# Kernel optimization log

Hardware: AMD Instinct MI355X
Metric: run time of the kernel (lower is better)

Reference implementation:

```python
import jax, jax.numpy as jnp
import numpy as np

R, DIL = 3, 2  # radius, dilation for neighbor correlation


def conv2d(x, w, b):
    # standard 3x3 stride-1 SAME conv, NCHW / OIHW
    y = jax.lax.conv_general_dilated(x, w, (1, 1), 'SAME',
                                     dimension_numbers=('NCHW', 'OIHW', 'NCHW'))
    return y + b[None, :, None, None]


def bilinear_gather(x, py, px):
    # x: (n,c,h,w); py/px: (n,K,h,w) float sampling coords; zero outside bounds
    n, c, h, w = x.shape
    y0 = jnp.floor(py); x0 = jnp.floor(px)
    wy = py - y0; wx = px - x0
    xf = x.reshape(n, c, h * w)

    def gather(yi, xi):
        valid = ((yi >= 0) & (yi < h) & (xi >= 0) & (xi < w)).astype(x.dtype)
        yc = jnp.clip(yi, 0, h - 1).astype(jnp.int32)
        xc = jnp.clip(xi, 0, w - 1).astype(jnp.int32)
        idx = (yc * w + xc).reshape(n, -1)  # (n, K*h*w)
        v = jax.vmap(lambda f, i: f[:, i])(xf, idx)  # (n, c, K*h*w)
        return v.reshape(n, c, *yi.shape[1:]) * valid[:, None]

    v00 = gather(y0, x0); v01 = gather(y0, x0 + 1)
    v10 = gather(y0 + 1, x0); v11 = gather(y0 + 1, x0 + 1)
    wy_ = wy[:, None]; wx_ = wx[:, None]
    return (v00 * (1 - wy_) * (1 - wx_) + v01 * (1 - wy_) * wx_
            + v10 * wy_ * (1 - wx_) + v11 * wy_ * wx_)


def dcn(x, w, b, ow, ob):
    # DCNv2-style modulated deformable 3x3 conv, stride 1, pad 1, 1 deformable group.
    # Offset/mask predicted by an internal conv: channels = [dy(9), dx(9), mask(9)].
    n, c, h, w_ = x.shape
    K = 9
    om = conv2d(x, ow, ob)  # (n, 27, h, w)
    dy, dx = om[:, :K], om[:, K:2 * K]
    mask = jax.nn.sigmoid(om[:, 2 * K:])
    ky, kx = jnp.meshgrid(jnp.arange(-1, 2), jnp.arange(-1, 2), indexing='ij')
    ky = ky.reshape(K).astype(x.dtype); kx = kx.reshape(K).astype(x.dtype)
    yy = jnp.arange(h, dtype=x.dtype)[None, None, :, None]
    xx = jnp.arange(w_, dtype=x.dtype)[None, None, None, :]
    py = yy + ky[None, :, None, None] + dy  # (n,K,h,w)
    px = xx + kx[None, :, None, None] + dx
    samp = bilinear_gather(x, py, px) * mask[:, None]  # (n,c,K,h,w)
    return jnp.einsum('nckhw,ock->nohw', samp, w.reshape(w.shape[0], c, K)) + b[None, :, None, None]


def ncf(f1, f2, radius, dilation):
    # neighbor_correlation_filter: unfold-based sliding-window dot-product attention
    n, c, h, w = f2.shape
    k = 2 * radius + 1
    pad = (k - 1) * dilation // 2
    f2p = jnp.pad(f2, ((0, 0), (0, 0), (pad, pad), (pad, pad)))
    # (n,c,K,h,w), tap order (ky outer, kx inner) matching F.unfold row-major layout
    patches = jnp.stack([f2p[:, :, i * dilation:i * dilation + h, j * dilation:j * dilation + w]
                         for i in range(k) for j in range(k)], axis=2)
    corr = jnp.einsum('nchw,nckhw->nkhw', f1, patches) / jnp.sqrt(jnp.asarray(c, f1.dtype))
    attn = jax.nn.softmax(corr, axis=1)
    sample = jnp.einsum('nkhw,nckhw->nchw', attn, patches)
    return sample, corr


def stargru(x, t, zw, zb, zow, zob, hw, hb, how, hob):
    tx = jnp.concatenate([x, t], axis=1)
    z = jax.nn.sigmoid(dcn(tx, zw, zb, zow, zob))
    r, _ = ncf(t, x, R, DIL)
    xt = jnp.tanh(dcn(jnp.concatenate([r, t], axis=1), hw, hb, how, hob))
    return (1.0 - z) * t + z * xt


def setup_inputs():
    key = jax.random.key(0)
    N, CIN, CH, H, W = 2, 256, 64, 96, 96
    ks = iter(jax.random.split(key, 32))

    def rn(shape, s=0.05):
        return jax.random.normal(next(ks), shape, jnp.float32) * s

    inp = {
        'x': jax.random.normal(next(ks), (N, CIN, H, W), jnp.float32),
        'template': jax.random.normal(next(ks), (N, CH, H, W), jnp.float32),
        'w_in': rn((CH, CIN, 3, 3)), 'b_in': jnp.zeros((CH,), jnp.float32),
        'w_out': rn((CIN, CH, 3, 3)), 'b_out': jnp.zeros((CIN,), jnp.float32),
    }
    for pre in ('enh_z', 'enh_h', 'upd_z', 'upd_h'):
        inp[pre + '_w'] = rn((CH, 2 * CH, 3, 3))
        inp[pre + '_b'] = jnp.zeros((CH,), jnp.float32)
        inp[pre + '_ow'] = rn((27, 2 * CH, 3, 3), 0.01)  # offset/mask conv (small init)
        inp[pre + '_ob'] = jnp.zeros((27,), jnp.float32)
    return inp


def reference(x, template, w_in, b_in, w_out, b_out,
              enh_z_w, enh_z_b, enh_z_ow, enh_z_ob,
              enh_h_w, enh_h_b, enh_h_ow, enh_h_ob,
              upd_z_w, upd_z_b, upd_z_ow, upd_z_ob,
              upd_h_w, upd_h_b, upd_h_ow, upd_h_ob):
    # CrossUpdate forward, post-first-frame branch (self.template is not None)
    xh = conv2d(x, w_in, b_in)
    x_enh = stargru(template, xh,
                    enh_z_w, enh_z_b, enh_z_ow, enh_z_ob,
                    enh_h_w, enh_h_b, enh_h_ow, enh_h_ob)
    new_template = stargru(xh, template,
                           upd_z_w, upd_z_b, upd_z_ow, upd_z_ob,
                           upd_h_w, upd_h_b, upd_h_ow, upd_h_ob)
    out = conv2d(x_enh, w_out, b_out)
    return (out, new_template)
```

## Files before the change

### kernel.cpp

```cpp
#include <hip/hip_runtime.h>
#include <hip/hip_bf16.h>

typedef __hip_bfloat16 bf16;
typedef unsigned short u16;
typedef unsigned int u32;
typedef __attribute__((ext_vector_type(8))) short short8;
typedef __attribute__((ext_vector_type(4))) short bh4;
typedef __attribute__((ext_vector_type(4))) float floatx4;

constexpr int N_ = 2, H_ = 96, W_ = 96, HW_ = H_ * W_;
constexpr int CIN_ = 256, CH_ = 64, C2_ = 128;

__device__ __forceinline__ float sigm(float v) { return 1.0f / (1.0f + __expf(-v)); }
__device__ __forceinline__ short f2b(float v) { bf16 h = __float2bfloat16(v); return *reinterpret_cast<short*>(&h); }
__device__ __forceinline__ float b2f(short s) {
    union { u32 i; float f; } v; v.i = ((u32)(u16)s) << 16; return v.f;
}

constexpr int A_IN_OFF = 0,                         A_IN_SZ  = 64 * 2304;
constexpr int A_OUT_OFF = A_IN_OFF + A_IN_SZ,       A_OUT_SZ = 256 * 576;
constexpr int A_OFF_OFF = A_OUT_OFF + A_OUT_SZ,     A_OFF_SZ = 64 * 1152;
constexpr int A_DCN_OFF = A_OFF_OFF + 4 * A_OFF_SZ, A_DCN_SZ = 64 * 1152;
constexpr int A_TOT = A_DCN_OFF + 4 * A_DCN_SZ;

__global__ __launch_bounds__(256) void cvt_weights(
        const float* __restrict__ w_in, const float* __restrict__ w_out,
        const float* __restrict__ ow0, const float* __restrict__ ow1,
        const float* __restrict__ ow2, const float* __restrict__ ow3,
        const float* __restrict__ w0, const float* __restrict__ w1,
        const float* __restrict__ w2, const float* __restrict__ w3,
        u16* __restrict__ dst) {
    int id = blockIdx.x * 256 + threadIdx.x;
    if (id >= A_TOT) return;
    float v;
    if (id < A_OUT_OFF) {
        int l = id; int m = l / 2304, k = l % 2304; int tap = k >> 8, ic = k & 255;
        v = w_in[m * 2304 + ic * 9 + tap];
    } else if (id < A_OFF_OFF) {
        int l = id - A_OUT_OFF; int m = l / 576, k = l % 576; int tap = k / 64, ic = k & 63;
        v = w_out[m * 576 + ic * 9 + tap];
    } else if (id < A_DCN_OFF) {
        int l = id - A_OFF_OFF; int i = l / A_OFF_SZ, l2 = l % A_OFF_SZ;
        int m = l2 / 1152, k = l2 % 1152; int tap = k >> 7, ic = k & 127;
        const float* s = (i == 0) ? ow0 : (i == 1) ? ow1 : (i == 2) ? ow2 : ow3;
        v = (m < 27) ? s[m * 1152 + ic * 9 + tap] : 0.f;
    } else {
        int l = id - A_DCN_OFF; int i = l / A_DCN_SZ, l2 = l % A_DCN_SZ;
        int m = l2 / 1152, k = l2 % 1152; int tap = k >> 7, c = k & 127;
        const float* s = (i == 0) ? w0 : (i == 1) ? w1 : (i == 2) ? w2 : w3;
        v = s[m * 1152 + c * 9 + tap];
    }
    short sb = f2b(v);
    dst[id] = *reinterpret_cast<u16*>(&sb);
}

__global__ __launch_bounds__(256) void prep(const float* __restrict__ x, const float* __restrict__ tpl,
                                            u16* __restrict__ xT, u16* __restrict__ ta, u16* __restrict__ tb) {
    int id = blockIdx.x * 256 + threadIdx.x;
    constexpr int XIDS = N_ * HW_ * 32;
    if (id < XIDS) {
        int c8 = id & 31;
        int pix = id >> 5;
        int n = pix / HW_, p = pix % HW_;
        const float* s = x + ((size_t)n * 256 + c8 * 8) * HW_ + p;
        short8 vv;
#pragma unroll
        for (int j = 0; j < 8; ++j) vv[j] = f2b(s[(size_t)j * HW_]);
        *reinterpret_cast<short8*>(xT + (size_t)pix * 256 + c8 * 8) = vv;
    } else {
        int id2 = id - XIDS;
        int c8 = id2 & 7;
        int pix = id2 >> 3;
        int n = pix / HW_, p = pix % HW_;
        const float* s = tpl + ((size_t)n * 64 + c8 * 8) * HW_ + p;
        short8 vv;
#pragma unroll
        for (int j = 0; j < 8; ++j) vv[j] = f2b(s[(size_t)j * HW_]);
        *reinterpret_cast<short8*>(ta + (size_t)pix * 128 + c8 * 8) = vv;
        *reinterpret_cast<short8*>(tb + (size_t)pix * 128 + 64 + c8 * 8) = vv;
    }
}

template <int IC, int OCST, int CC>
__device__ __forceinline__ void conv_core(const u16* __restrict__ X,
                                          const u16* __restrict__ A,
                                          const float* __restrict__ bias,
                                          float* __restrict__ out,
                                          u16* __restrict__ ta, u16* __restrict__ tb,
                                          int r, int mt, int t) {
    constexpr int K = IC * 9;
    constexpr int ICC = IC / 64;
    __shared__ __align__(16) u16 Xl[3][50][72];
    int n = r / 192;
    int rr = r % 192;
    int y = rr >> 1, px0 = (rr & 1) * 48;
    int w = t >> 6, lane = t & 63, lm = lane & 15, q = lane >> 4;
    const u16* Arow = A + (size_t)(mt * 64 + w * 16 + lm) * K + q * 8;
    floatx4 acc[3];
#pragma unroll
    for (int a = 0; a < 3; ++a) acc[a] = {0.f, 0.f, 0.f, 0.f};
    const short8 zz = {0, 0, 0, 0, 0, 0, 0, 0};

    for (int icc = 0; icc < ICC; ++icc) {
        short8 af[9][2];
#pragma unroll
        for (int tap = 0; tap < 9; ++tap)
#pragma unroll
            for (int ks = 0; ks < 2; ++ks)
                af[tap][ks] = *reinterpret_cast<const short8*>(Arow + tap * IC + icc * 64 + ks * 32);
        __syncthreads();
#pragma unroll
        for (int it = 0; it < 5; ++it) {
            int id = it * 256 + t;
            if (id < 1200) {
                int ch8 = id & 7;
                int tmp = id >> 3;
                int pxl = tmp % 50, row = tmp / 50;
                int xg = px0 - 1 + pxl;
                int yg = y - 1 + row;
                bool vld = (yg >= 0) && (yg < 96) && (xg >= 0) && (xg < 96);
                short8 vv = zz;
                if (vld)
                    vv = *reinterpret_cast<const short8*>(
                        X + ((size_t)(n * HW_ + yg * 96 + xg)) * IC + icc * 64 + ch8 * 8);
                *reinterpret_cast<short8*>(&Xl[row][pxl][ch8 * 8]) = vv;
            }
        }
        __syncthreads();
#pragma unroll
        for (int tap = 0; tap < 9; ++tap) {
            int ky = tap / 3, kx = tap % 3;
#pragma unroll
            for (int ks = 0; ks < 2; ++ks) {
#pragma unroll
                for (int nf = 0; nf < 3; ++nf) {
                    short8 bv = *reinterpret_cast<const short8*>(&Xl[ky][nf * 16 + lm + kx][ks * 32 + q * 8]);
                    acc[nf] = __builtin_amdgcn_mfma_f32_16x16x32_bf16(af[tap][ks], bv, acc[nf], 0, 0, 0);
                }
            }
        }
    }
    int ocb = mt * 64 + w * 16 + q * 4;
#pragma unroll
    for (int nf = 0; nf < 3; ++nf) {
        int px = px0 + nf * 16 + lm;
        if constexpr (CC) {
            int pix = n * HW_ + y * 96 + px;
            bh4 bo;
#pragma unroll
            for (int rr2 = 0; rr2 < 4; ++rr2) {
                int oc = ocb + rr2;
                float v = acc[nf][rr2] + bias[oc];
                out[((size_t)(n * OCST + oc)) * HW_ + y * 96 + px] = v;
                bo[rr2] = f2b(v);
            }
            *reinterpret_cast<bh4*>(ta + (size_t)pix * 128 + 64 + ocb) = bo;
            *reinterpret_cast<bh4*>(tb + (size_t)pix * 128 + ocb) = bo;
        } else {
#pragma unroll
            for (int rr2 = 0; rr2 < 4; ++rr2) {
                int oc = ocb + rr2;
                if (oc < OCST)
                    out[((size_t)(n * OCST + oc)) * HW_ + y * 96 + px] = acc[nf][rr2] + bias[oc];
            }
        }
    }
}

template <int IC, int OCST, int CC>
__global__ __launch_bounds__(256) void conv_gemm(const u16* __restrict__ X,
                                                 const u16* __restrict__ A,
                                                 const float* __restrict__ bias,
                                                 float* __restrict__ out,
                                                 u16* __restrict__ ta, u16* __restrict__ tb) {
    int cpx = gridDim.x >> 3;
    int b = (blockIdx.x & 7) * cpx + (blockIdx.x >> 3);
    conv_core<IC, OCST, CC>(X, A, bias, out, ta, tb, b % 384, b / 384, threadIdx.x);
}

template <int GATE>
__global__ __launch_bounds__(256) void od_fused(
        const u16* __restrict__ X0, const u16* __restrict__ X1,
        const u16* __restrict__ Ao0, const u16* __restrict__ Ao1,
        const float* __restrict__ bo0, const float* __restrict__ bo1,
        const u16* __restrict__ Ad0, const u16* __restrict__ Ad1,
        const float* __restrict__ bd0, const float* __restrict__ bd1,
        float* __restrict__ o0, float* __restrict__ o1,
        const float* __restrict__ g0, const float* __restrict__ g1,
        const float* __restrict__ t0, const float* __restrict__ t1,
        u16* __restrict__ xeh, float* __restrict__ ontpl) {
    __shared__ __align__(16) u16 Xl[3][50][72];
    __shared__ float om_l[27][48];
    __shared__ __align__(16) u16 Bl[2][48][72];
    __shared__ float s_wy[432], s_wx[432], s_m[432];
    __shared__ int s_y0[432], s_x0[432];

    int bid = blockIdx.x;
    int b = (bid & 7) * 96 + (bid >> 3);
    int inst = b / 384, r = b % 384, t = threadIdx.x;
    const u16* X = inst ? X1 : X0;
    const u16* Ao = inst ? Ao1 : Ao0;
    const float* bo = inst ? bo1 : bo0;
    const u16* Ad = inst ? Ad1 : Ad0;
    const float* bd = inst ? bd1 : bd0;
    int n = r / 192, rr = r % 192;
    int y = rr >> 1, px0 = (rr & 1) * 48;
    int w = t >> 6, lane = t & 63, lm = lane & 15, q = lane >> 4;
    const short8 zz = {0, 0, 0, 0, 0, 0, 0, 0};

    {
        const u16* Arow = Ao + (size_t)(w * 16 + lm) * 1152 + q * 8;
        floatx4 acc[3];
#pragma unroll
        for (int a = 0; a < 3; ++a) acc[a] = {0.f, 0.f, 0.f, 0.f};
        for (int icc = 0; icc < 2; ++icc) {
            short8 af[9][2];
#pragma unroll
            for (int tap = 0; tap < 9; ++tap)
#pragma unroll
                for (int ks = 0; ks < 2; ++ks)
                    af[tap][ks] = *reinterpret_cast<const short8*>(Arow + tap * 128 + icc * 64 + ks * 32);
            __syncthreads();
#pragma unroll
            for (int it = 0; it < 5; ++it) {
                int id = it * 256 + t;
                if (id < 1200) {
                    int ch8 = id & 7;
                    int tmp = id >> 3;
                    int pxl = tmp % 50, row = tmp / 50;
                    int xg = px0 - 1 + pxl;
                    int yg = y - 1 + row;
                    bool vld = (yg >= 0) && (yg < 96) && (xg >= 0) && (xg < 96);
                    short8 vv = zz;
                    if (vld)
                        vv = *reinterpret_cast<const short8*>(
                            X + ((size_t)(n * HW_ + yg * 96 + xg)) * 128 + icc * 64 + ch8 * 8);
                    *reinterpret_cast<short8*>(&Xl[row][pxl][ch8 * 8]) = vv;
                }
            }
            __syncthreads();
#pragma unroll
            for (int tap = 0; tap < 9; ++tap) {
                int ky = tap / 3, kx = tap % 3;
#pragma unroll
                for (int ks = 0; ks < 2; ++ks) {
#pragma unroll
                    for (int nf = 0; nf < 3; ++nf) {
                        short8 bv = *reinterpret_cast<const short8*>(&Xl[ky][nf * 16 + lm + kx][ks * 32 + q * 8]);
                        acc[nf] = __builtin_amdgcn_mfma_f32_16x16x32_bf16(af[tap][ks], bv, acc[nf], 0, 0, 0);
                    }
                }
            }
        }
        int ocb = w * 16 + q * 4;
#pragma unroll
        for (int nf = 0; nf < 3; ++nf) {
            int xl = nf * 16 + lm;
#pragma unroll
            for (int rr2 = 0; rr2 < 4; ++rr2) {
                int oc = ocb + rr2;
                if (oc < 27) om_l[oc][xl] = acc[nf][rr2] + bo[oc];
            }
        }
    }
    __syncthreads();

    for (int e = t; e < 432; e += 256) {
        int k9 = e / 48, xl = e % 48;
        int x = px0 + xl;
        float dy = om_l[k9][xl];
        float dx = om_l[9 + k9][xl];
        float ml = om_l[18 + k9][xl];
        float py = (float)y + (float)(k9 / 3 - 1) + dy;
        float px = (float)x + (float)(k9 % 3 - 1) + dx;
        float fy = floorf(py), fx = floorf(px);
        s_y0[e] = (int)fy; s_x0[e] = (int)fx;
        s_wy[e] = py - fy; s_wx[e] = px - fx; s_m[e] = sigm(ml);
    }
    __syncthreads();

    const u16* Arow = Ad + (size_t)(w * 16 + lm) * 1152 + q * 8;
    floatx4 acc[3];
#pragma unroll
    for (int a = 0; a < 3; ++a) acc[a] = {0.f, 0.f, 0.f, 0.f};
    const u16* txn = X + (size_t)n * HW_ * 128;
    int p = 0;
    bool active = (t < 192);
    short8 cA[4], cB[4];
    short8 afP[2];

    auto issueI = [&](int kc_, int id, short8* cr) {
        int tap = kc_ >> 1, c0 = (kc_ & 1) * 64;
        int px = id >> 3, ch8 = id & 7;
        int ce = tap * 48 + px;
        int y0 = s_y0[ce], x0c = s_x0[ce];
        bool yv0 = (y0 >= 0) & (y0 < 96), yv1 = (y0 >= -1) & (y0 < 95);
        bool xv0 = (x0c >= 0) & (x0c < 96), xv1 = (x0c >= -1) & (x0c < 95);
        const u16* gb = txn + (long)(y0 * 96 + x0c) * 128 + c0 + ch8 * 8;
        cr[0] = (yv0 && xv0) ? *reinterpret_cast<const short8*>(gb) : zz;
        cr[1] = (yv0 && xv1) ? *reinterpret_cast<const short8*>(gb + 128) : zz;
        cr[2] = (yv1 && xv0) ? *reinterpret_cast<const short8*>(gb + 96 * 128) : zz;
        cr[3] = (yv1 && xv1) ? *reinterpret_cast<const short8*>(gb + 96 * 128 + 128) : zz;
    };
    auto computeI = [&](int kc_, int id, const short8* cr) {
        int tap = kc_ >> 1;
        int px = id >> 3, ch8 = id & 7;
        int ce = tap * 48 + px;
        float wy = s_wy[ce], wx = s_wx[ce], m = s_m[ce];
        float w00 = (1.f - wy) * (1.f - wx) * m;
        float w01 = (1.f - wy) * wx * m;
        float w10 = wy * (1.f - wx) * m;
        float w11 = wy * wx * m;
        short8 vv;
#pragma unroll
        for (int j = 0; j < 8; ++j) {
            float f = b2f(cr[0][j]) * w00 + b2f(cr[1][j]) * w01 +
                      b2f(cr[2][j]) * w10 + b2f(cr[3][j]) * w11;
            vv[j] = f2b(f);
        }
        *reinterpret_cast<short8*>(&Bl[p][px][ch8 * 8]) = vv;
    };

    if (active) { issueI(0, t, cA); issueI(0, t + 192, cB); }
    for (int kc = 0; kc < 18; ++kc) {
        if (kc > 0) {
#pragma unroll
            for (int ks = 0; ks < 2; ++ks)
#pragma unroll
                for (int nf = 0; nf < 3; ++nf) {
                    short8 bv = *reinterpret_cast<const short8*>(&Bl[p ^ 1][nf * 16 + lm][ks * 32 + q * 8]);
                    acc[nf] = __builtin_amdgcn_mfma_f32_16x16x32_bf16(afP[ks], bv, acc[nf], 0, 0, 0);
                }
        }
        if (active) {
            computeI(kc, t, cA);
            computeI(kc, t + 192, cB);
            if (kc < 17) { issueI(kc + 1, t, cA); issueI(kc + 1, t + 192, cB); }
        }
#pragma unroll
        for (int ks = 0; ks < 2; ++ks)
            afP[ks] = *reinterpret_cast<const short8*>(Arow + kc * 64 + ks * 32);
        __syncthreads();
        p ^= 1;
    }
#pragma unroll
    for (int ks = 0; ks < 2; ++ks)
#pragma unroll
        for (int nf = 0; nf < 3; ++nf) {
            short8 bv = *reinterpret_cast<const short8*>(&Bl[p ^ 1][nf * 16 + lm][ks * 32 + q * 8]);
            acc[nf] = __builtin_amdgcn_mfma_f32_16x16x32_bf16(afP[ks], bv, acc[nf], 0, 0, 0);
        }

    int ocb = w * 16 + q * 4;
    if constexpr (GATE == 0) {
        float* out = inst ? o1 : o0;
#pragma unroll
        for (int nf = 0; nf < 3; ++nf) {
            int px = px0 + nf * 16 + lm;
#pragma unroll
            for (int rr2 = 0; rr2 < 4; ++rr2) {
                int oc = ocb + rr2;
                out[((size_t)(n * CH_ + oc)) * HW_ + y * 96 + px] = acc[nf][rr2] + bd[oc];
            }
        }
    } else {
        const float* gz = inst ? g1 : g0;
        const float* tt = inst ? t1 : t0;
#pragma unroll
        for (int nf = 0; nf < 3; ++nf) {
            int px = px0 + nf * 16 + lm;
            if (!inst) {
                bh4 bo4;
#pragma unroll
                for (int rr2 = 0; rr2 < 4; ++rr2) {
                    int oc = ocb + rr2;
                    size_t idx = ((size_t)(n * CH_ + oc)) * HW_ + y * 96 + px;
                    float z = sigm(gz[idx]);
                    float xt = tanhf(acc[nf][rr2] + bd[oc]);
                    bo4[rr2] = f2b((1.f - z) * tt[idx] + z * xt);
                }
                *reinterpret_cast<bh4*>(xeh + ((size_t)(n * HW_ + y * 96 + px)) * 64 + ocb) = bo4;
            } else {
#pragma unroll
                for (int rr2 = 0; rr2 < 4; ++rr2) {
                    int oc = ocb + rr2;
                    size_t idx = ((size_t)(n * CH_ + oc)) * HW_ + y * 96 + px;
                    float z = sigm(gz[idx]);
                    float xt = tanhf(acc[nf][rr2] + bd[oc]);
                    ontpl[idx] = (1.f - z) * tt[idx] + z * xt;
                }
            }
        }
    }
}

__global__ __launch_bounds__(256, 4) void ncf2(const u16* __restrict__ in0, const u16* __restrict__ in1,
                                               u16* __restrict__ out0, u16* __restrict__ out1) {
    __shared__ __align__(16) u16 sF2[7][28][72];
    __shared__ __align__(16) u16 sF1[16][72];
    __shared__ float sc[16][52];
    int t = threadIdx.x;
    int bid = blockIdx.x;
    int b = (bid & 7) * 288 + (bid >> 3);
    int inst = b / 1152, bb = b % 1152;
    const u16* txh = inst ? in1 : in0;
    u16* txh2 = inst ? out1 : out0;
    int n = bb / 576, rem = bb % 576;
    int y = rem / 6, x0 = (rem % 6) * 16;
    const u16* base = txh + (size_t)n * HW_ * 128;
    const short8 zz = {0, 0, 0, 0, 0, 0, 0, 0};

    for (int id = t; id < 1568; id += 256) {
        int ch8 = id & 7;
        int tmp = id >> 3;
        int px = tmp % 28, row = tmp / 28;
        int yy = y + row * 2 - 6;
        int xg = x0 - 6 + px;
        short8 vv = zz;
        if (yy >= 0 && yy < 96 && xg >= 0 && xg < 96)
            vv = *reinterpret_cast<const short8*>(base + (size_t)(yy * 96 + xg) * 128 + ch8 * 8);
        *reinterpret_cast<short8*>(&sF2[row][px][ch8 * 8]) = vv;
    }
    if (t < 128) {
        int ch8 = t & 7, lp0 = t >> 3;
        short8 vv = *reinterpret_cast<const short8*>(base + (size_t)(y * 96 + x0 + lp0) * 128 + 64 + ch8 * 8);
        *reinterpret_cast<short8*>(&sF1[lp0][ch8 * 8]) = vv;
    }
    __syncthreads();

    int lp = t >> 4, j = t & 15;
    for (int k = j; k < 49; k += 16) {
        int ky = k / 7, kx = k % 7;
        const u16* f2p = &sF2[ky][lp + 2 * kx][0];
        const u16* f1p = &sF1[lp][0];
        float s = 0.f;
#pragma unroll
        for (int c8 = 0; c8 < 8; ++c8) {
            short8 a = *reinterpret_cast<const short8*>(f1p + c8 * 8);
            short8 b2 = *reinterpret_cast<const short8*>(f2p + c8 * 8);
#pragma unroll
            for (int u = 0; u < 8; ++u) s += b2f(a[u]) * b2f(b2[u]);
        }
        sc[lp][k] = s * 0.125f;
    }
    float mx = -1e30f;
    for (int k = j; k < 49; k += 16) mx = fmaxf(mx, sc[lp][k]);
#pragma unroll
    for (int m = 1; m <= 8; m <<= 1) mx = fmaxf(mx, __shfl_xor(mx, m, 64));
    float e[4];
    float sum = 0.f;
    int cnt = 0;
    for (int k = j; k < 49; k += 16) { e[cnt] = __expf(sc[lp][k] - mx); sum += e[cnt]; ++cnt; }
#pragma unroll
    for (int m = 1; m <= 8; m <<= 1) sum += __shfl_xor(sum, m, 64);
    float inv = 1.f / sum;
    cnt = 0;
    for (int k = j; k < 49; k += 16) sc[lp][k] = e[cnt++] * inv;
    __syncthreads();
    int ch0 = j * 4;
    float acc[4];
#pragma unroll
    for (int u = 0; u < 4; ++u) acc[u] = 0.f;
#pragma unroll
    for (int k = 0; k < 49; ++k) {
        int ky = k / 7, kx = k % 7;
        float a = sc[lp][k];
        bh4 f2 = *reinterpret_cast<const bh4*>(&sF2[ky][lp + 2 * kx][ch0]);
#pragma unroll
        for (int u = 0; u < 4; ++u) acc[u] += a * b2f(f2[u]);
    }
    int p = y * 96 + x0 + lp;
    u16* obase = txh2 + (size_t)n * HW_ * 128 + (size_t)p * 128;
    bh4 ro;
#pragma unroll
    for (int u = 0; u < 4; ++u) ro[u] = f2b(acc[u]);
    *reinterpret_cast<bh4*>(obase + ch0) = ro;
    *reinterpret_cast<bh4*>(obase + 64 + ch0) =
        *reinterpret_cast<const bh4*>(&sF1[lp][ch0]);
}

extern "C" void kernel_launch(void* const* d_in, const int* in_sizes, int n_in,
                              void* d_out, int out_size, void* d_ws, size_t ws_size,
                              hipStream_t stream) {
    const float* x     = (const float*)d_in[0];
    const float* tpl   = (const float*)d_in[1];
    const float* w_in  = (const float*)d_in[2];
    const float* b_in  = (const float*)d_in[3];
    const float* w_out = (const float*)d_in[4];
    const float* b_out = (const float*)d_in[5];
    const float *pw[4], *pb[4], *pow_[4], *pob[4];
    for (int i = 0; i < 4; ++i) {
        pw[i]   = (const float*)d_in[6 + 4 * i];
        pb[i]   = (const float*)d_in[7 + 4 * i];
        pow_[i] = (const float*)d_in[8 + 4 * i];
        pob[i]  = (const float*)d_in[9 + 4 * i];
    }
    float* out_main = (float*)d_out;
    float* out_ntpl = out_main + (size_t)N_ * CIN_ * HW_;

    u16* Aws = (u16*)d_ws;
    u16* xT     = Aws + A_TOT;
    u16* txh_a  = xT + (size_t)N_ * HW_ * CIN_;
    u16* txh_b  = txh_a + (size_t)N_ * HW_ * C2_;
    u16* txh2_a = txh_b + (size_t)N_ * HW_ * C2_;
    u16* txh2_b = txh2_a + (size_t)N_ * HW_ * C2_;
    u16* xeh    = txh2_b + (size_t)N_ * HW_ * C2_;
    float* fws = (float*)(xeh + (size_t)N_ * HW_ * CH_);
    size_t off = 0;
    float* xh   = fws + off; off += (size_t)N_ * CH_ * HW_;
    float* dz_a = fws + off; off += (size_t)N_ * CH_ * HW_;
    float* dz_b = fws + off; off += (size_t)N_ * CH_ * HW_;

    cvt_weights<<<(A_TOT + 255) / 256, 256, 0, stream>>>(
        w_in, w_out, pow_[0], pow_[1], pow_[2], pow_[3], pw[0], pw[1], pw[2], pw[3], Aws);
    prep<<<2880, 256, 0, stream>>>(x, tpl, xT, txh_a, txh_b);
    conv_gemm<CIN_, 64, 1><<<384, 256, 0, stream>>>(xT, Aws + A_IN_OFF, b_in, xh, txh_a, txh_b);

    od_fused<0><<<768, 256, 0, stream>>>(txh_a, txh_b,
        Aws + A_OFF_OFF + 0 * A_OFF_SZ, Aws + A_OFF_OFF + 2 * A_OFF_SZ, pob[0], pob[2],
        Aws + A_DCN_OFF + 0 * A_DCN_SZ, Aws + A_DCN_OFF + 2 * A_DCN_SZ, pb[0], pb[2],
        dz_a, dz_b, nullptr, nullptr, nullptr, nullptr, nullptr, nullptr);

    ncf2<<<2304, 256, 0, stream>>>(txh_a, txh_b, txh2_a, txh2_b);

    od_fused<1><<<768, 256, 0, stream>>>(txh2_a, txh2_b,
        Aws + A_OFF_OFF + 1 * A_OFF_SZ, Aws + A_OFF_OFF + 3 * A_OFF_SZ, pob[1], pob[3],
        Aws + A_DCN_OFF + 1 * A_DCN_SZ, Aws + A_DCN_OFF + 3 * A_DCN_SZ, pb[1], pb[3],
        nullptr, nullptr, dz_a, dz_b, xh, tpl, xeh, out_ntpl);

    conv_gemm<CH_, 256, 0><<<1536, 256, 0, stream>>>(xeh, Aws + A_OUT_OFF, b_out, out_main, nullptr, nullptr);
}
```

Before: 310.6 us.

## Shrink pixel tile to 32 to raise block count and alias shared memory

Changes the per-block pixel tile from 48 to 32 pixels in the conv and fused offset/DCN kernels, raising grid sizes by half so more blocks spread across the CUs. In od_fused, the shared buffers are merged into one aliased allocation (the conv-stage input tile and the later B tile share storage), which lowers LDS use per block and can raise occupancy. All 256 threads now take part in the bilinear gather instead of 192 with two items each. The cost is more halo reloads and more weight-fragment reloads per output pixel.

```diff
diff --git a/kernel.cpp b/kernel.cpp
--- a/kernel.cpp
+++ b/kernel.cpp
@@ -90,15 +90,15 @@
                                           int r, int mt, int t) {
     constexpr int K = IC * 9;
     constexpr int ICC = IC / 64;
-    __shared__ __align__(16) u16 Xl[3][50][72];
-    int n = r / 192;
-    int rr = r % 192;
-    int y = rr >> 1, px0 = (rr & 1) * 48;
+    __shared__ __align__(16) u16 Xl[3][34][72];
+    int n = r / 288;
+    int rr = r % 288;
+    int y = rr / 3, px0 = (rr % 3) * 32;
     int w = t >> 6, lane = t & 63, lm = lane & 15, q = lane >> 4;
     const u16* Arow = A + (size_t)(mt * 64 + w * 16 + lm) * K + q * 8;
-    floatx4 acc[3];
-#pragma unroll
-    for (int a = 0; a < 3; ++a) acc[a] = {0.f, 0.f, 0.f, 0.f};
+    floatx4 acc[2];
+#pragma unroll
+    for (int a = 0; a < 2; ++a) acc[a] = {0.f, 0.f, 0.f, 0.f};
     const short8 zz = {0, 0, 0, 0, 0, 0, 0, 0};
 
     for (int icc = 0; icc < ICC; ++icc) {
@@ -110,12 +110,12 @@
                 af[tap][ks] = *reinterpret_cast<const short8*>(Arow + tap * IC + icc * 64 + ks * 32);
         __syncthreads();
 #pragma unroll
-        for (int it = 0; it < 5; ++it) {
+        for (int it = 0; it < 4; ++it) {
             int id = it * 256 + t;
-            if (id < 1200) {
+            if (id < 816) {
                 int ch8 = id & 7;
                 int tmp = id >> 3;
-                int pxl = tmp % 50, row = tmp / 50;
+                int pxl = tmp % 34, row = tmp / 34;
                 int xg = px0 - 1 + pxl;
                 int yg = y - 1 + row;
                 bool vld = (yg >= 0) && (yg < 96) && (xg >= 0) && (xg < 96);
@@ -133,7 +133,7 @@
 #pragma unroll
             for (int ks = 0; ks < 2; ++ks) {
 #pragma unroll
-                for (int nf = 0; nf < 3; ++nf) {
+                for (int nf = 0; nf < 2; ++nf) {
                     short8 bv = *reinterpret_cast<const short8*>(&Xl[ky][nf * 16 + lm + kx][ks * 32 + q * 8]);
                     acc[nf] = __builtin_amdgcn_mfma_f32_16x16x32_bf16(af[tap][ks], bv, acc[nf], 0, 0, 0);
                 }
@@ -142,7 +142,7 @@
     }
     int ocb = mt * 64 + w * 16 + q * 4;
 #pragma unroll
-    for (int nf = 0; nf < 3; ++nf) {
+    for (int nf = 0; nf < 2; ++nf) {
         int px = px0 + nf * 16 + lm;
         if constexpr (CC) {
             int pix = n * HW_ + y * 96 + px;
@@ -175,8 +175,14 @@
                                                  u16* __restrict__ ta, u16* __restrict__ tb) {
     int cpx = gridDim.x >> 3;
     int b = (blockIdx.x & 7) * cpx + (blockIdx.x >> 3);
-    conv_core<IC, OCST, CC>(X, A, bias, out, ta, tb, b % 384, b / 384, threadIdx.x);
-}
+    conv_core<IC, OCST, CC>(X, A, bias, out, ta, tb, b % 576, b / 576, threadIdx.x);
+}
+
+constexpr int XL_B  = 3 * 34 * 72 * 2;
+constexpr int OM_B  = 27 * 32 * 4;
+constexpr int P1_B  = XL_B + OM_B;
+constexpr int S_B   = 288 * 5 * 4;
+constexpr int SM_SZ2 = P1_B + S_B;
 
 template <int GATE>
 __global__ __launch_bounds__(256) void od_fused(
@@ -189,30 +195,34 @@
         const float* __restrict__ g0, const float* __restrict__ g1,
         const float* __restrict__ t0, const float* __restrict__ t1,
         u16* __restrict__ xeh, float* __restrict__ ontpl) {
-    __shared__ __align__(16) u16 Xl[3][50][72];
-    __shared__ float om_l[27][48];
-    __shared__ __align__(16) u16 Bl[2][48][72];
-    __shared__ float s_wy[432], s_wx[432], s_m[432];
-    __shared__ int s_y0[432], s_x0[432];
+    __shared__ __align__(16) char smem[SM_SZ2];
+    u16 (*Xl)[34][72] = reinterpret_cast<u16(*)[34][72]>(smem);
+    float (*om_l)[32] = reinterpret_cast<float(*)[32]>(smem + XL_B);
+    u16 (*Bl)[32][72] = reinterpret_cast<u16(*)[32][72]>(smem);
+    int* s_y0 = reinterpret_cast<int*>(smem + P1_B);
+    int* s_x0 = s_y0 + 288;
+    float* s_wy = reinterpret_cast<float*>(s_x0 + 288);
+    float* s_wx = s_wy + 288;
+    float* s_m  = s_wx + 288;
 
     int bid = blockIdx.x;
-    int b = (bid & 7) * 96 + (bid >> 3);
-    int inst = b / 384, r = b % 384, t = threadIdx.x;
+    int b = (bid & 7) * 144 + (bid >> 3);
+    int inst = b / 576, r = b % 576, t = threadIdx.x;
     const u16* X = inst ? X1 : X0;
     const u16* Ao = inst ? Ao1 : Ao0;
     const float* bo = inst ? bo1 : bo0;
     const u16* Ad = inst ? Ad1 : Ad0;
     const float* bd = inst ? bd1 : bd0;
-    int n = r / 192, rr = r % 192;
-    int y = rr >> 1, px0 = (rr & 1) * 48;
+    int n = r / 288, rr = r % 288;
+    int y = rr / 3, px0 = (rr % 3) * 32;
     int w = t >> 6, lane = t & 63, lm = lane & 15, q = lane >> 4;
     const short8 zz = {0, 0, 0, 0, 0, 0, 0, 0};
 
     {
         const u16* Arow = Ao + (size_t)(w * 16 + lm) * 1152 + q * 8;
-        floatx4 acc[3];
-#pragma unroll
-        for (int a = 0; a < 3; ++a) acc[a] = {0.f, 0.f, 0.f, 0.f};
+        floatx4 acc[2];
+#pragma unroll
+        for (int a = 0; a < 2; ++a) acc[a] = {0.f, 0.f, 0.f, 0.f};
         for (int icc = 0; icc < 2; ++icc) {
             short8 af[9][2];
 #pragma unroll
@@ -222,12 +232,12 @@
                     af[tap][ks] = *reinterpret_cast<const short8*>(Arow + tap * 128 + icc * 64 + ks * 32);
             __syncthreads();
 #pragma unroll
-            for (int it = 0; it < 5; ++it) {
+            for (int it = 0; it < 4; ++it) {
                 int id = it * 256 + t;
-                if (id < 1200) {
+                if (id < 816) {
                     int ch8 = id & 7;
                     int tmp = id >> 3;
-                    int pxl = tmp % 50, row = tmp / 50;
+                    int pxl = tmp % 34, row = tmp / 34;
                     int xg = px0 - 1 + pxl;
                     int yg = y - 1 + row;
                     bool vld = (yg >= 0) && (yg < 96) && (xg >= 0) && (xg < 96);
@@ -245,7 +255,7 @@
 #pragma unroll
                 for (int ks = 0; ks < 2; ++ks) {
 #pragma unroll
-                    for (int nf = 0; nf < 3; ++nf) {
+                    for (int nf = 0; nf < 2; ++nf) {
                         short8 bv = *reinterpret_cast<const short8*>(&Xl[ky][nf * 16 + lm + kx][ks * 32 + q * 8]);
                         acc[nf] = __builtin_amdgcn_mfma_f32_16x16x32_bf16(af[tap][ks], bv, acc[nf], 0, 0, 0);
                     }
@@ -254,7 +264,7 @@
         }
         int ocb = w * 16 + q * 4;
 #pragma unroll
-        for (int nf = 0; nf < 3; ++nf) {
+        for (int nf = 0; nf < 2; ++nf) {
             int xl = nf * 16 + lm;
 #pragma unroll
             for (int rr2 = 0; rr2 < 4; ++rr2) {
@@ -265,8 +275,8 @@
     }
     __syncthreads();
 
-    for (int e = t; e < 432; e += 256) {
-        int k9 = e / 48, xl = e % 48;
+    for (int e = t; e < 288; e += 256) {
+        int k9 = e >> 5, xl = e & 31;
         int x = px0 + xl;
         float dy = om_l[k9][xl];
         float dx = om_l[9 + k9][xl];
@@ -280,32 +290,30 @@
     __syncthreads();
 
     const u16* Arow = Ad + (size_t)(w * 16 + lm) * 1152 + q * 8;
-    floatx4 acc[3];
-#pragma unroll
-    for (int a = 0; a < 3; ++a) acc[a] = {0.f, 0.f, 0.f, 0.f};
+    floatx4 acc[2];
+#pragma unroll
+    for (int a = 0; a < 2; ++a) acc[a] = {0.f, 0.f, 0.f, 0.f};
     const u16* txn = X + (size_t)n * HW_ * 128;
     int p = 0;
-    bool active = (t < 192);
-    short8 cA[4], cB[4];
+    int pxi = t >> 3, ch8 = t & 7;
+    short8 cA[4];
     short8 afP[2];
 
-    auto issueI = [&](int kc_, int id, short8* cr) {
+    auto issueI = [&](int kc_) {
         int tap = kc_ >> 1, c0 = (kc_ & 1) * 64;
-        int px = id >> 3, ch8 = id & 7;
-        int ce = tap * 48 + px;
+        int ce = tap * 32 + pxi;
         int y0 = s_y0[ce], x0c = s_x0[ce];
         bool yv0 = (y0 >= 0) & (y0 < 96), yv1 = (y0 >= -1) & (y0 < 95);
         bool xv0 = (x0c >= 0) & (x0c < 96), xv1 = (x0c >= -1) & (x0c < 95);
         const u16* gb = txn + (long)(y0 * 96 + x0c) * 128 + c0 + ch8 * 8;
-        cr[0] = (yv0 && xv0) ? *reinterpret_cast<const short8*>(gb) : zz;
-        cr[1] = (yv0 && xv1) ? *reinterpret_cast<const short8*>(gb + 128) : zz;
-        cr[2] = (yv1 && xv0) ? *reinterpret_cast<const short8*>(gb + 96 * 128) : zz;
-        cr[3] = (yv1 && xv1) ? *reinterpret_cast<const short8*>(gb + 96 * 128 + 128) : zz;
+        cA[0] = (yv0 && xv0) ? *reinterpret_cast<const short8*>(gb) : zz;
+        cA[1] = (yv0 && xv1) ? *reinterpret_cast<const short8*>(gb + 128) : zz;
+        cA[2] = (yv1 && xv0) ? *reinterpret_cast<const short8*>(gb + 96 * 128) : zz;
+        cA[3] = (yv1 && xv1) ? *reinterpret_cast<const short8*>(gb + 96 * 128 + 128) : zz;
     };
-    auto computeI = [&](int kc_, int id, const short8* cr) {
+    auto computeI = [&](int kc_) {
         int tap = kc_ >> 1;
-        int px = id >> 3, ch8 = id & 7;
-        int ce = tap * 48 + px;
+        int ce = tap * 32 + pxi;
         float wy = s_wy[ce], wx = s_wx[ce], m = s_m[ce];
         float w00 = (1.f - wy) * (1.f - wx) * m;
         float w01 = (1.f - wy) * wx * m;
@@ -314,29 +322,26 @@
         short8 vv;
 #pragma unroll
         for (int j = 0; j < 8; ++j) {
-            float f = b2f(cr[0][j]) * w00 + b2f(cr[1][j]) * w01 +
-                      b2f(cr[2][j]) * w10 + b2f(cr[3][j]) * w11;
+            float f = b2f(cA[0][j]) * w00 + b2f(cA[1][j]) * w01 +
+                      b2f(cA[2][j]) * w10 + b2f(cA[3][j]) * w11;
             vv[j] = f2b(f);
         }
-        *reinterpret_cast<short8*>(&Bl[p][px][ch8 * 8]) = vv;
+        *reinterpret_cast<short8*>(&Bl[p][pxi][ch8 * 8]) = vv;
     };
 
-    if (active) { issueI(0, t, cA); issueI(0, t + 192, cB); }
+    issueI(0);
     for (int kc = 0; kc < 18; ++kc) {
         if (kc > 0) {
 #pragma unroll
             for (int ks = 0; ks < 2; ++ks)
 #pragma unroll
-                for (int nf = 0; nf < 3; ++nf) {
+                for (int nf = 0; nf < 2; ++nf) {
                     short8 bv = *reinterpret_cast<const short8*>(&Bl[p ^ 1][nf * 16 + lm][ks * 32 + q * 8]);
                     acc[nf] = __builtin_amdgcn_mfma_f32_16x16x32_bf16(afP[ks], bv, acc[nf], 0, 0, 0);
                 }
         }
-        if (active) {
-            computeI(kc, t, cA);
-            computeI(kc, t + 192, cB);
-            if (kc < 17) { issueI(kc + 1, t, cA); issueI(kc + 1, t + 192, cB); }
-        }
+        computeI(kc);
+        if (kc < 17) issueI(kc + 1);
 #pragma unroll
         for (int ks = 0; ks < 2; ++ks)
             afP[ks] = *reinterpret_cast<const short8*>(Arow + kc * 64 + ks * 32);
@@ -346,7 +351,7 @@
 #pragma unroll
     for (int ks = 0; ks < 2; ++ks)
 #pragma unroll
-        for (int nf = 0; nf < 3; ++nf) {
+        for (int nf = 0; nf < 2; ++nf) {
             short8 bv = *reinterpret_cast<const short8*>(&Bl[p ^ 1][nf * 16 + lm][ks * 32 + q * 8]);
             acc[nf] = __builtin_amdgcn_mfma_f32_16x16x32_bf16(afP[ks], bv, acc[nf], 0, 0, 0);
         }
@@ -355,7 +360,7 @@
     if constexpr (GATE == 0) {
         float* out = inst ? o1 : o0;
 #pragma unroll
-        for (int nf = 0; nf < 3; ++nf) {
+        for (int nf = 0; nf < 2; ++nf) {
             int px = px0 + nf * 16 + lm;
 #pragma unroll
             for (int rr2 = 0; rr2 < 4; ++rr2) {
@@ -367,7 +372,7 @@
         const float* gz = inst ? g1 : g0;
         const float* tt = inst ? t1 : t0;
 #pragma unroll
-        for (int nf = 0; nf < 3; ++nf) {
+        for (int nf = 0; nf < 2; ++nf) {
             int px = px0 + nf * 16 + lm;
             if (!inst) {
                 bh4 bo4;
@@ -514,19 +519,19 @@
     cvt_weights<<<(A_TOT + 255) / 256, 256, 0, stream>>>(
         w_in, w_out, pow_[0], pow_[1], pow_[2], pow_[3], pw[0], pw[1], pw[2], pw[3], Aws);
     prep<<<2880, 256, 0, stream>>>(x, tpl, xT, txh_a, txh_b);
-    conv_gemm<CIN_, 64, 1><<<384, 256, 0, stream>>>(xT, Aws + A_IN_OFF, b_in, xh, txh_a, txh_b);
-
-    od_fused<0><<<768, 256, 0, stream>>>(txh_a, txh_b,
+    conv_gemm<CIN_, 64, 1><<<576, 256, 0, stream>>>(xT, Aws + A_IN_OFF, b_in, xh, txh_a, txh_b);
+
+    od_fused<0><<<1152, 256, 0, stream>>>(txh_a, txh_b,
         Aws + A_OFF_OFF + 0 * A_OFF_SZ, Aws + A_OFF_OFF + 2 * A_OFF_SZ, pob[0], pob[2],
         Aws + A_DCN_OFF + 0 * A_DCN_SZ, Aws + A_DCN_OFF + 2 * A_DCN_SZ, pb[0], pb[2],
         dz_a, dz_b, nullptr, nullptr, nullptr, nullptr, nullptr, nullptr);
 
     ncf2<<<2304, 256, 0, stream>>>(txh_a, txh_b, txh2_a, txh2_b);
 
-    od_fused<1><<<768, 256, 0, stream>>>(txh2_a, txh2_b,
+    od_fused<1><<<1152, 256, 0, stream>>>(txh2_a, txh2_b,
         Aws + A_OFF_OFF + 1 * A_OFF_SZ, Aws + A_OFF_OFF + 3 * A_OFF_SZ, pob[1], pob[3],
         Aws + A_DCN_OFF + 1 * A_DCN_SZ, Aws + A_DCN_OFF + 3 * A_DCN_SZ, pb[1], pb[3],
         nullptr, nullptr, dz_a, dz_b, xh, tpl, xeh, out_ntpl);
 
-    conv_gemm<CH_, 256, 0><<<1536, 256, 0, stream>>>(xeh, Aws + A_OUT_OFF, b_out, out_main, nullptr, nullptr);
-}
+    conv_gemm<CH_, 256, 0><<<2304, 256, 0, stream>>>(xeh, Aws + A_OUT_OFF, b_out, out_main, nullptr, nullptr);
+}
```

Measured after the change: 347.2 us. 11.8% more time.

## Gather full 128-channel tap per stage in deformable conv with aliased shared memory

Applied to the files above, without the earlier changes.

The deformable sampling loop now processes one full tap (all 128 channels) per pipeline stage, giving 9 stages instead of 18. All 256 threads take part in the gather, each handling three pixels of one 8-channel group, where before only 192 threads were active. Shared buffers are packed into one aliased byte array so the phase-1 input tile and the double-buffered B tile share storage. Launch bounds now request 4 blocks per SM, so fewer barriers and more gather parallelism come at the cost of higher register pressure from 12 in-flight short8 loads per thread.

```diff
diff --git a/kernel.cpp b/kernel.cpp
--- a/kernel.cpp
+++ b/kernel.cpp
@@ -178,8 +178,12 @@
     conv_core<IC, OCST, CC>(X, A, bias, out, ta, tb, b % 384, b / 384, threadIdx.x);
 }
 
+constexpr int P1XL_B = 21600;
+constexpr int P1_B   = 26784;
+constexpr int SM_SZ2 = 35424;
+
 template <int GATE>
-__global__ __launch_bounds__(256) void od_fused(
+__global__ __launch_bounds__(256, 4) void od_fused(
         const u16* __restrict__ X0, const u16* __restrict__ X1,
         const u16* __restrict__ Ao0, const u16* __restrict__ Ao1,
         const float* __restrict__ bo0, const float* __restrict__ bo1,
@@ -189,11 +193,15 @@
         const float* __restrict__ g0, const float* __restrict__ g1,
         const float* __restrict__ t0, const float* __restrict__ t1,
         u16* __restrict__ xeh, float* __restrict__ ontpl) {
-    __shared__ __align__(16) u16 Xl[3][50][72];
-    __shared__ float om_l[27][48];
-    __shared__ __align__(16) u16 Bl[2][48][72];
-    __shared__ float s_wy[432], s_wx[432], s_m[432];
-    __shared__ int s_y0[432], s_x0[432];
+    __shared__ __align__(16) char smem[SM_SZ2];
+    u16 (*Xl)[50][72] = reinterpret_cast<u16(*)[50][72]>(smem);
+    float (*om_l)[48] = reinterpret_cast<float(*)[48]>(smem + P1XL_B);
+    u16 (*Bl)[48][136] = reinterpret_cast<u16(*)[48][136]>(smem);
+    int* s_y0 = reinterpret_cast<int*>(smem + P1_B);
+    int* s_x0 = s_y0 + 432;
+    float* s_wy = reinterpret_cast<float*>(s_x0 + 432);
+    float* s_wx = s_wy + 432;
+    float* s_m  = s_wx + 432;
 
     int bid = blockIdx.x;
     int b = (bid & 7) * 96 + (bid >> 3);
@@ -285,71 +293,80 @@
     for (int a = 0; a < 3; ++a) acc[a] = {0.f, 0.f, 0.f, 0.f};
     const u16* txn = X + (size_t)n * HW_ * 128;
     int p = 0;
-    bool active = (t < 192);
-    short8 cA[4], cB[4];
-    short8 afP[2];
-
-    auto issueI = [&](int kc_, int id, short8* cr) {
-        int tap = kc_ >> 1, c0 = (kc_ & 1) * 64;
-        int px = id >> 3, ch8 = id & 7;
-        int ce = tap * 48 + px;
-        int y0 = s_y0[ce], x0c = s_x0[ce];
-        bool yv0 = (y0 >= 0) & (y0 < 96), yv1 = (y0 >= -1) & (y0 < 95);
-        bool xv0 = (x0c >= 0) & (x0c < 96), xv1 = (x0c >= -1) & (x0c < 95);
-        const u16* gb = txn + (long)(y0 * 96 + x0c) * 128 + c0 + ch8 * 8;
-        cr[0] = (yv0 && xv0) ? *reinterpret_cast<const short8*>(gb) : zz;
-        cr[1] = (yv0 && xv1) ? *reinterpret_cast<const short8*>(gb + 128) : zz;
-        cr[2] = (yv1 && xv0) ? *reinterpret_cast<const short8*>(gb + 96 * 128) : zz;
-        cr[3] = (yv1 && xv1) ? *reinterpret_cast<const short8*>(gb + 96 * 128 + 128) : zz;
+    int cg = t & 15, px0i = t >> 4;
+    short8 cr[3][4];
+    short8 afP[2][2];
+
+    auto issueT = [&](int tap) {
+#pragma unroll
+        for (int s = 0; s < 3; ++s) {
+            int pxi = px0i + s * 16;
+            int ce = tap * 48 + pxi;
+            int y0 = s_y0[ce], x0c = s_x0[ce];
+            bool yv0 = (y0 >= 0) & (y0 < 96), yv1 = (y0 >= -1) & (y0 < 95);
+            bool xv0 = (x0c >= 0) & (x0c < 96), xv1 = (x0c >= -1) & (x0c < 95);
+            const u16* gb = txn + (long)(y0 * 96 + x0c) * 128 + cg * 8;
+            cr[s][0] = (yv0 && xv0) ? *reinterpret_cast<const short8*>(gb) : zz;
+            cr[s][1] = (yv0 && xv1) ? *reinterpret_cast<const short8*>(gb + 128) : zz;
+            cr[s][2] = (yv1 && xv0) ? *reinterpret_cast<const short8*>(gb + 96 * 128) : zz;
+            cr[s][3] = (yv1 && xv1) ? *reinterpret_cast<const short8*>(gb + 96 * 128 + 128) : zz;
+        }
     };
-    auto computeI = [&](int kc_, int id, const short8* cr) {
-        int tap = kc_ >> 1;
-        int px = id >> 3, ch8 = id & 7;
-        int ce = tap * 48 + px;
-        float wy = s_wy[ce], wx = s_wx[ce], m = s_m[ce];
-        float w00 = (1.f - wy) * (1.f - wx) * m;
-        float w01 = (1.f - wy) * wx * m;
-        float w10 = wy * (1.f - wx) * m;
-        float w11 = wy * wx * m;
-        short8 vv;
-#pragma unroll
-        for (int j = 0; j < 8; ++j) {
-            float f = b2f(cr[0][j]) * w00 + b2f(cr[1][j]) * w01 +
-                      b2f(cr[2][j]) * w10 + b2f(cr[3][j]) * w11;
-            vv[j] = f2b(f);
-        }
-        *reinterpret_cast<short8*>(&Bl[p][px][ch8 * 8]) = vv;
+    auto computeT = [&](int tap) {
+#pragma unroll
+        for (int s = 0; s < 3; ++s) {
+            int pxi = px0i + s * 16;
+            int ce = tap * 48 + pxi;
+            float wy = s_wy[ce], wx = s_wx[ce], m = s_m[ce];
+            float w00 = (1.f - wy) * (1.f - wx) * m;
+            float w01 = (1.f - wy) * wx * m;
+            float w10 = wy * (1.f - wx) * m;
+            float w11 = wy * wx * m;
+            short8 vv;
+#pragma unroll
+            for (int j = 0; j < 8; ++j) {
+                float f = b2f(cr[s][0][j]) * w00 + b2f(cr[s][1][j]) * w01 +
+                          b2f(cr[s][2][j]) * w10 + b2f(cr[s][3][j]) * w11;
+                vv[j] = f2b(f);
+            }
+            *reinterpret_cast<short8*>(&Bl[p][pxi][cg * 8]) = vv;
+        }
     };
 
-    if (active) { issueI(0, t, cA); issueI(0, t + 192, cB); }
-    for (int kc = 0; kc < 18; ++kc) {
-        if (kc > 0) {
+    issueT(0);
+    for (int tap = 0; tap < 9; ++tap) {
+        if (tap > 0) {
+#pragma unroll
+            for (int half = 0; half < 2; ++half)
+#pragma unroll
+                for (int ks = 0; ks < 2; ++ks)
+#pragma unroll
+                    for (int nf = 0; nf < 3; ++nf) {
+                        short8 bv = *reinterpret_cast<const short8*>(
+                            &Bl[p ^ 1][nf * 16 + lm][half * 64 + ks * 32 + q * 8]);
+                        acc[nf] = __builtin_amdgcn_mfma_f32_16x16x32_bf16(afP[half][ks], bv, acc[nf], 0, 0, 0);
+                    }
+        }
+        computeT(tap);
+        if (tap < 8) issueT(tap + 1);
+#pragma unroll
+        for (int half = 0; half < 2; ++half)
 #pragma unroll
             for (int ks = 0; ks < 2; ++ks)
-#pragma unroll
-                for (int nf = 0; nf < 3; ++nf) {
-                    short8 bv = *reinterpret_cast<const short8*>(&Bl[p ^ 1][nf * 16 + lm][ks * 32 + q * 8]);
-                    acc[nf] = __builtin_amdgcn_mfma_f32_16x16x32_bf16(afP[ks], bv, acc[nf], 0, 0, 0);
-                }
-        }
-        if (active) {
-            computeI(kc, t, cA);
-            computeI(kc, t + 192, cB);
-            if (kc < 17) { issueI(kc + 1, t, cA); issueI(kc + 1, t + 192, cB); }
-        }
-#pragma unroll
-        for (int ks = 0; ks < 2; ++ks)
-            afP[ks] = *reinterpret_cast<const short8*>(Arow + kc * 64 + ks * 32);
+                afP[half][ks] = *reinterpret_cast<const short8*>(Arow + (tap * 2 + half) * 64 + ks * 32);
         __syncthreads();
         p ^= 1;
     }
 #pragma unroll
-    for (int ks = 0; ks < 2; ++ks)
-#pragma unroll
-        for (int nf = 0; nf < 3; ++nf) {
-            short8 bv = *reinterpret_cast<const short8*>(&Bl[p ^ 1][nf * 16 + lm][ks * 32 + q * 8]);
-            acc[nf] = __builtin_amdgcn_mfma_f32_16x16x32_bf16(afP[ks], bv, acc[nf], 0, 0, 0);
-        }
+    for (int half = 0; half < 2; ++half)
+#pragma unroll
+        for (int ks = 0; ks < 2; ++ks)
+#pragma unroll
+            for (int nf = 0; nf < 3; ++nf) {
+                short8 bv = *reinterpret_cast<const short8*>(
+                    &Bl[p ^ 1][nf * 16 + lm][half * 64 + ks * 32 + q * 8]);
+                acc[nf] = __builtin_amdgcn_mfma_f32_16x16x32_bf16(afP[half][ks], bv, acc[nf], 0, 0, 0);
+            }
 
     int ocb = w * 16 + q * 4;
     if constexpr (GATE == 0) {
```

New measurement: 306.5 us. No clear change (-1.3%).
